# Kernel tuning notes

Measured on AMD Instinct MI355X. Metric: run time of the kernel, lower is better.

Reference implementation:

```python
import jax, jax.numpy as jnp
import numpy as np

Nu, Ni, Nb, Nc, Nr = 100000, 100000, 5000, 2000, 50000
E, Eb, Ec, Er = 600000, 100000, 200000, 400000
D, L = 64, 50


def _seg_softmax(logits, seg, n):
    m = jax.ops.segment_max(logits, seg, num_segments=n)
    e = jnp.exp(logits - m[seg])
    s = jax.ops.segment_sum(e, seg, num_segments=n)
    return e / (s[seg] + 1e-9)


def setup_inputs():
    key = jax.random.key(0)
    ks = jax.random.split(key, 32)
    f = lambda i, shape, s=0.05: jax.random.normal(ks[i], shape, jnp.float32) * s
    return dict(
        user_h=f(0, (Nu, D), 1.0), item_h=f(1, (Ni, D), 1.0),
        brand_feat=f(2, (Nb, D), 1.0), cat_feat=f(3, (Nc, D), 1.0), rel_feat=f(4, (Nr, D), 1.0),
        Wu=f(5, (D, D)), Wi=f(6, (D, D)), Wb=f(7, (D, D)), Wc=f(8, (D, D)), Wr=f(9, (D, D)),
        Wg_u=f(10, (2 * D, D)), Wg_i=f(11, (2 * D, D)),
        u_pos=f(12, (L, D)), u_pos_k=f(13, (L, D)), i_pos=f(14, (L, D)), i_pos_k=f(15, (L, D)),
        basis_freq=jnp.asarray(1.0 / 10 ** np.linspace(0, 9, D), jnp.float32),
        phase=jnp.zeros((D,), jnp.float32),
        Wr0=f(16, (D, D)), Wr1=f(17, (D, D)), Wr2=f(18, (D, D)),
        e_time=jax.random.uniform(ks[19], (E,), jnp.float32),
        e_iid=jax.random.randint(ks[20], (E,), 0, Ni),
        e_uid=jax.random.randint(ks[21], (E,), 0, Nu),
        pos_u=jax.random.randint(ks[22], (E,), 0, L),
        pos_i=jax.random.randint(ks[23], (E,), 0, L),
        eb_src=jax.random.randint(ks[24], (Eb,), 0, Nb),
        eb_dst=jax.random.randint(ks[25], (Eb,), 0, Ni),
        ec_src=jax.random.randint(ks[26], (Ec,), 0, Nc),
        ec_dst=jax.random.randint(ks[27], (Ec,), 0, Ni),
        er_src=jax.random.randint(ks[28], (Er,), 0, Nr),
        er_dst=jax.random.randint(ks[29], (Er,), 0, Ni),
    )


def reference(user_h, item_h, brand_feat, cat_feat, rel_feat, Wu, Wi, Wb, Wc, Wr,
              Wg_u, Wg_i, u_pos, u_pos_k, i_pos, i_pos_k, basis_freq, phase,
              Wr0, Wr1, Wr2, e_time,
              e_iid, e_uid, pos_u, pos_i, eb_src, eb_dst, ec_src, ec_dst, er_src, er_dst):
    sqrtD = jnp.sqrt(jnp.float32(D))
    # relation-specific linear transforms (user_weight / item_weight / att_trans)
    uh = user_h @ Wu                      # [Nu,D]
    ih = item_h @ Wi                      # [Ni,D]
    bf = brand_feat @ Wb
    cf = cat_feat @ Wc
    rf = rel_feat @ Wr
    # TimeEncode harmonic features per purchase edge
    t_enc = jnp.cos(e_time[:, None] * basis_freq[None, :] + phase[None, :])  # [E,D]

    hi = ih[e_iid]                        # [E,D] item-side gather
    hu = uh[e_uid]                        # [E,D] user-side gather

    # ---- user aggregation: 'orgat' long-term (pos + time aware) + 'att' short-term ----
    k_long = hi + u_pos_k[pos_u] + t_enc
    a_long = _seg_softmax(jnp.sum(k_long * hu, -1) / sqrtD, e_uid, Nu)
    h_long_u = jax.ops.segment_sum(a_long[:, None] * (hi + u_pos[pos_u]), e_uid, num_segments=Nu)
    a_short = _seg_softmax(jnp.sum(hi * hu, -1) / sqrtD, e_uid, Nu)
    h_short_u = jax.ops.segment_sum(a_short[:, None] * hi, e_uid, num_segments=Nu)
    user_new = jnp.concatenate([h_long_u, h_short_u], -1) @ Wg_u  # agg_gate_u

    # ---- item aggregation from users (symmetric) ----
    k_long_i = hu + i_pos_k[pos_i] + t_enc
    b_long = _seg_softmax(jnp.sum(k_long_i * hi, -1) / sqrtD, e_iid, Ni)
    h_long_i = jax.ops.segment_sum(b_long[:, None] * (hu + i_pos[pos_i]), e_iid, num_segments=Ni)
    b_short = _seg_softmax(jnp.sum(hu * hi, -1) / sqrtD, e_iid, Ni)
    h_short_i = jax.ops.segment_sum(b_short[:, None] * hu, e_iid, num_segments=Ni)
    item_new = jnp.concatenate([h_long_i, h_short_i], -1) @ Wg_i  # agg_gate_i

    # ---- relation mean aggregation onto items (reduce_trans per relation) ----
    def mean_agg(feat, src, dst, W):
        s = jax.ops.segment_sum(feat[src], dst, num_segments=Ni)
        c = jax.ops.segment_sum(jnp.ones(src.shape, feat.dtype), dst, num_segments=Ni)
        return (s / jnp.maximum(c, 1.0)[:, None]) @ W

    item_new = item_new + mean_agg(bf, eb_src, eb_dst, Wr0) \
                        + mean_agg(cf, ec_src, ec_dst, Wr1) \
                        + mean_agg(rf, er_src, er_dst, Wr2)

    # residual update: elu(now + old)
    user_out = jax.nn.elu(user_new + user_h)
    item_out = jax.nn.elu(item_new + item_h)
    return user_out, item_out
```

## Files before the change

### kernel.cpp

```cpp
#include <hip/hip_runtime.h>
#include <hip/hip_bf16.h>
#include <hip/hip_fp16.h>

typedef __hip_bfloat16 bf16_t;

#define NU 100000
#define NI 100000
#define NB_ 5000
#define NC_ 2000
#define NR_ 50000
#define NE 600000
#define NEB 100000
#define NEC 200000
#define NER 400000
#define NPERM (2 * NE + NEB + NEC + NER)
#define NRELE (NEB + NEC + NER)
#define NALL (NE + NRELE)
#define SCAN_N (2 * NU + NI + 1)
#define SCAN_CHUNK 2048
#define SCAN_NCHUNK ((SCAN_N + SCAN_CHUNK - 1) / SCAN_CHUNK)
#define PBLK 8192
#define RBLK ((NRELE + 255) / 256)

#define AGS 136
#define RLS 68

typedef __attribute__((ext_vector_type(8))) short short8;
typedef __attribute__((ext_vector_type(4))) short short4v;
typedef __attribute__((ext_vector_type(4))) float f32x4;

__device__ __forceinline__ float b2f(bf16_t x) { return __bfloat162float(x); }
__device__ __forceinline__ float sane(float x) { return isfinite(x) ? x : 0.f; }
__device__ __forceinline__ unsigned short f2bu(float x) {
    union { bf16_t b; unsigned short u; } c; c.b = __float2bfloat16(x); return c.u;
}

__device__ __forceinline__ float ldf(const void* p, size_t i, int f32) {
    return f32 ? ((const float*)p)[i] : __bfloat162float(((const bf16_t*)p)[i]);
}
__device__ __forceinline__ void stf(void* p, size_t i, float v, int f32) {
    if (f32) ((float*)p)[i] = v;
    else     ((bf16_t*)p)[i] = __float2bfloat16(v);
}

__device__ __forceinline__ f32x4 bf4(const bf16_t* p) {
    short4v s = *(const short4v*)p;
    f32x4 r;
#pragma unroll
    for (int q = 0; q < 4; ++q)
        r[q] = __uint_as_float(((unsigned)(unsigned short)s[q]) << 16);
    return r;
}
__device__ __forceinline__ f32x4 ldf4(const void* p, size_t i, int f32) {
    if (f32) return *(const f32x4*)((const float*)p + i);
    return bf4((const bf16_t*)p + i);
}

__device__ __forceinline__ void bf8(const bf16_t* p, float* o) {
    short8 s = *(const short8*)p;
#pragma unroll
    for (int q = 0; q < 8; ++q)
        o[q] = __uint_as_float(((unsigned)(unsigned short)s[q]) << 16);
}
__device__ __forceinline__ void ldf8(const void* p, size_t i, int f32, float* o) {
    if (f32) {
        f32x4 a = *(const f32x4*)((const float*)p + i);
        f32x4 b = *(const f32x4*)((const float*)p + i + 4);
#pragma unroll
        for (int q = 0; q < 4; ++q) { o[q] = a[q]; o[4 + q] = b[q]; }
    } else {
        bf8((const bf16_t*)p + i, o);
    }
}

__global__ void detect_dtype(const unsigned int* w, int* flag) {
    if (threadIdx.x == 0 && blockIdx.x == 0) *flag = (w[0] == 0x3F800000u) ? 1 : 0;
}

__global__ __launch_bounds__(256) void combine_w(
    const void* Wb, const void* Wr0,
    const void* Wc, const void* Wr1,
    const void* Wr, const void* Wr2,
    const void* Wg_u, const void* Wg_i,
    bf16_t* out, bf16_t* wgsw, const int* flagp) {
    int f = *flagp;
    if (blockIdx.x < 48) {
        int mat = blockIdx.x >> 4;
        int sub = blockIdx.x & 15;
        const void* A = mat == 0 ? Wb : (mat == 1 ? Wc : Wr);
        const void* B = mat == 0 ? Wr0 : (mat == 1 ? Wr1 : Wr2);
        int idx = sub * 256 + threadIdx.x;
        int i = idx >> 6, j = idx & 63;
        float acc = 0.f;
        for (int k = 0; k < 64; ++k)
            acc = fmaf(ldf(A, i * 64 + k, f), ldf(B, k * 64 + j, f), acc);
        out[(size_t)mat * 4096 + idx] = __float2bfloat16(acc);
    } else {
        int t = (blockIdx.x - 48) * 256 + threadIdx.x;
        int mat = t >> 13;
        int i = t & 8191;
        int j = i & 7, ln = (i >> 3) & 63, p = i >> 9;
        int kk4 = p >> 2, n0t = p & 3;
        int srow = kk4 * 32 + (ln >> 4) * 8 + j;
        int scol = n0t * 16 + (ln & 15);
        const void* src = mat ? Wg_i : Wg_u;
        wgsw[(size_t)mat * 8192 + i] = __float2bfloat16(ldf(src, (size_t)srow * 64 + scol, f));
    }
}

struct GSeg {
    const void* A; const void* W; void* out;
    int M; int a_internal; int w_internal;
};

__global__ __launch_bounds__(256) void gemm_multi(
    GSeg s0, GSeg s1, GSeg s2, GSeg s3, GSeg s4,
    int nseg, const int* __restrict__ flagp) {
    const int K = 64;
    __shared__ short WL[64 * 64];
    int f = *flagp;
    int nt0 = (s0.M + 63) >> 6;
    int nt1 = (nseg > 1) ? ((s1.M + 63) >> 6) : 0;
    int nt2 = (nseg > 2) ? ((s2.M + 63) >> 6) : 0;
    int nt3 = (nseg > 3) ? ((s3.M + 63) >> 6) : 0;
    int nt4 = (nseg > 4) ? ((s4.M + 63) >> 6) : 0;
    int c0 = nt0, c1 = c0 + nt1, c2 = c1 + nt2, c3 = c2 + nt3;
    int ntT = c3 + nt4;
    int lane = threadIdx.x & 63;
    int wv = threadIdx.x >> 6;
    int q = lane >> 4, nl = lane & 15;
    int staged = -1;
    for (int tile = blockIdx.x; tile < ntT; tile += gridDim.x) {
        int sidx, t_in;
        if (tile < c0) { sidx = 0; t_in = tile; }
        else if (tile < c1) { sidx = 1; t_in = tile - c0; }
        else if (tile < c2) { sidx = 2; t_in = tile - c1; }
        else if (tile < c3) { sidx = 3; t_in = tile - c2; }
        else { sidx = 4; t_in = tile - c3; }
        const void* A; const void* W; void* out; int M, a_int, w_int;
        if (sidx == 0)      { A = s0.A; W = s0.W; out = s0.out; M = s0.M; a_int = s0.a_internal; w_int = s0.w_internal; }
        else if (sidx == 1) { A = s1.A; W = s1.W; out = s1.out; M = s1.M; a_int = s1.a_internal; w_int = s1.w_internal; }
        else if (sidx == 2) { A = s2.A; W = s2.W; out = s2.out; M = s2.M; a_int = s2.a_internal; w_int = s2.w_internal; }
        else if (sidx == 3) { A = s3.A; W = s3.W; out = s3.out; M = s3.M; a_int = s3.a_internal; w_int = s3.w_internal; }
        else                { A = s4.A; W = s4.W; out = s4.out; M = s4.M; a_int = s4.a_internal; w_int = s4.w_internal; }
        if (sidx != staged) {
            __syncthreads();
            int w_f32 = w_int ? 0 : f;
            for (int i = threadIdx.x; i < K * 64; i += 256) {
                int j = i & 7, ln = (i >> 3) & 63, p = i >> 9;
                int kk4 = p >> 2, n0t = p & 3;
                int srow = kk4 * 32 + (ln >> 4) * 8 + j;
                int scol = n0t * 16 + (ln & 15);
                float wvv = w_f32 ? ((const float*)W)[srow * 64 + scol]
                                  : b2f(((const bf16_t*)W)[srow * 64 + scol]);
                WL[i] = (short)f2bu(wvv);
            }
            __syncthreads();
            staged = sidx;
        }
        int m0 = t_in * 64 + wv * 16;
        if (m0 < M) {
            int a_f32 = a_int ? 0 : f;
            int arow = m0 + nl; if (arow >= M) arow = M - 1;
            f32x4 acc[4];
#pragma unroll
            for (int t = 0; t < 4; ++t) acc[t] = (f32x4){0.f, 0.f, 0.f, 0.f};
            for (int kk4 = 0; kk4 < 2; ++kk4) {
                short8 af;
                size_t abase = (size_t)arow * K + kk4 * 32 + q * 8;
                if (a_f32) {
                    const f32x4* ap = (const f32x4*)((const float*)A + abase);
                    f32x4 x0 = ap[0], x1 = ap[1];
#pragma unroll
                    for (int j = 0; j < 4; ++j) {
                        af[j] = (short)f2bu(x0[j]);
                        af[4 + j] = (short)f2bu(x1[j]);
                    }
                } else {
                    af = *(const short8*)((const bf16_t*)A + abase);
                }
#pragma unroll
                for (int n0t = 0; n0t < 4; ++n0t) {
                    short8 bfr = *(const short8*)&WL[(((kk4 << 2) + n0t) * 64 + lane) * 8];
                    acc[n0t] = __builtin_amdgcn_mfma_f32_16x16x32_bf16(af, bfr, acc[n0t], 0, 0, 0);
                }
            }
#pragma unroll
            for (int n0t = 0; n0t < 4; ++n0t) {
#pragma unroll
                for (int r = 0; r < 4; ++r) {
                    int row = m0 + q * 4 + r;
                    if (row >= M) continue;
                    int col = n0t * 16 + nl;
                    ((bf16_t*)out)[(size_t)row * 64 + col] = __float2bfloat16(acc[n0t][r]);
                }
            }
        }
    }
}

__global__ __launch_bounds__(256) void hist_all(
    const int* __restrict__ e_uid, const int* __restrict__ e_iid,
    const int* __restrict__ eb_dst, const int* __restrict__ ec_dst,
    const int* __restrict__ er_dst, int* __restrict__ deg) {
    int t = blockIdx.x * blockDim.x + threadIdx.x;
    if (t < NE) {
        atomicAdd(deg + e_uid[t], 1);
        atomicAdd(deg + NU + e_iid[t], 1);
    } else if (t < NE + NEB) {
        atomicAdd(deg + 2 * NU + eb_dst[t - NE], 1);
    } else if (t < NE + NEB + NEC) {
        atomicAdd(deg + 2 * NU + ec_dst[t - NE - NEB], 1);
    } else if (t < NALL) {
        atomicAdd(deg + 2 * NU + er_dst[t - NE - NEB - NEC], 1);
    }
}

__global__ __launch_bounds__(256) void scan1(const int* __restrict__ deg,
                                             int* __restrict__ off,
                                             int* __restrict__ ctot) {
    __shared__ int part[256];
    int base = blockIdx.x * SCAN_CHUNK + threadIdx.x * 8;
    int v[8]; int s = 0;
#pragma unroll
    for (int k = 0; k < 8; ++k) {
        int idx = base + k;
        v[k] = s;
        s += (idx < SCAN_N) ? deg[idx] : 0;
    }
    part[threadIdx.x] = s;
    __syncthreads();
    for (int o = 1; o < 256; o <<= 1) {
        int t = (threadIdx.x >= o) ? part[threadIdx.x - o] : 0;
        __syncthreads();
        part[threadIdx.x] += t;
        __syncthreads();
    }
    int texc = (threadIdx.x == 0) ? 0 : part[threadIdx.x - 1];
#pragma unroll
    for (int k = 0; k < 8; ++k) {
        int idx = base + k;
        if (idx < SCAN_N) off[idx] = texc + v[k];
    }
    if (threadIdx.x == 255) ctot[blockIdx.x] = part[255];
}
__global__ __launch_bounds__(256) void scan23(int* __restrict__ off,
                                              const int* __restrict__ ctot,
                                              int* __restrict__ cur) {
    __shared__ int part[256];
    int t = threadIdx.x;
    part[t] = (t < SCAN_NCHUNK) ? ctot[t] : 0;
    __syncthreads();
    for (int o = 1; o < 256; o <<= 1) {
        int x = (t >= o) ? part[t - o] : 0;
        __syncthreads();
        part[t] += x;
        __syncthreads();
    }
    int add = blockIdx.x ? part[blockIdx.x - 1] : 0;
    int base = blockIdx.x * SCAN_CHUNK + t;
#pragma unroll
    for (int k = 0; k < 8; ++k) {
        int idx = base + k * 256;
        if (idx < SCAN_N) { int v = off[idx] + add; off[idx] = v; cur[idx] = v; }
    }
}

__global__ __launch_bounds__(256) void edges_fused(
    const bf16_t* __restrict__ uh, const bf16_t* __restrict__ ih,
    const void* __restrict__ u_pos_k, const void* __restrict__ i_pos_k,
    const void* __restrict__ basis_freq, const void* __restrict__ phase_,
    const void* __restrict__ e_time,
    const int* __restrict__ e_uid, const int* __restrict__ e_iid,
    const int* __restrict__ pos_u, const int* __restrict__ pos_i,
    const int* __restrict__ eb_src, const int* __restrict__ eb_dst,
    const int* __restrict__ ec_src, const int* __restrict__ ec_dst,
    const int* __restrict__ er_src, const int* __restrict__ er_dst,
    int* __restrict__ cur, uint2* __restrict__ perm, const int* flagp) {
    if (blockIdx.x >= PBLK) {
        int t = (blockIdx.x - PBLK) * 256 + threadIdx.x;
        if (t < NEB) {
            int p = atomicAdd(cur + 2 * NU + eb_dst[t], 1);
            perm[p] = make_uint2((unsigned)eb_src[t], 0u);
        } else if (t < NEB + NEC) {
            int e = t - NEB;
            int p = atomicAdd(cur + 2 * NU + ec_dst[e], 1);
            perm[p] = make_uint2((unsigned)(ec_src[e] + NB_) | (1u << 17), 0u);
        } else if (t < NRELE) {
            int e = t - NEB - NEC;
            int p = atomicAdd(cur + 2 * NU + er_dst[e], 1);
            perm[p] = make_uint2((unsigned)(er_src[e] + NB_ + NC_) | (2u << 17), 0u);
        }
        return;
    }
    int f = *flagp;
    int lane = threadIdx.x & 63;
    int g = lane >> 3, l = lane & 7;
    float bfv[8], phv[8];
    ldf8(basis_freq, (size_t)l * 8, f, bfv);
    ldf8(phase_, (size_t)l * 8, f, phv);
    int w = (blockIdx.x * 256 + threadIdx.x) >> 6;
    const int NWAVE = PBLK * 4;
    for (int eb = w; eb < NE / 8; eb += NWAVE) {
        int e = eb * 8 + g;
        int uid = e_uid[e], iid = e_iid[e], pu = pos_u[e], pi = pos_i[e];
        float t = ldf(e_time, e, f);
        float hu[8], hi[8], pku[8], pki[8];
        bf8(uh + (size_t)uid * 64 + l * 8, hu);
        bf8(ih + (size_t)iid * 64 + l * 8, hi);
        ldf8(u_pos_k, (size_t)pu * 64 + l * 8, f, pku);
        ldf8(i_pos_k, (size_t)pi * 64 + l * 8, f, pki);
        float d_lu = 0.f, d_sh = 0.f, d_li = 0.f;
#pragma unroll
        for (int qq = 0; qq < 8; ++qq) {
            float te = __cosf(fmaf(t, bfv[qq], phv[qq]));
            d_lu = fmaf(hi[qq] + pku[qq] + te, hu[qq], d_lu);
            d_sh = fmaf(hi[qq], hu[qq], d_sh);
            d_li = fmaf(hu[qq] + pki[qq] + te, hi[qq], d_li);
        }
#pragma unroll
        for (int o = 1; o < 8; o <<= 1) {
            d_lu += __shfl_xor(d_lu, o, 64);
            d_sh += __shfl_xor(d_sh, o, 64);
            d_li += __shfl_xor(d_li, o, 64);
        }
        if (l == 0) {
            float p_lu = __expf(fminf(d_lu * 0.125f, 10.f));
            float p_sh = __expf(fminf(d_sh * 0.125f, 10.f));
            unsigned pkt_u = (unsigned)__half_as_ushort(__float2half(p_lu))
                           | ((unsigned)__half_as_ushort(__float2half(p_sh)) << 16);
            int s1 = atomicAdd(cur + uid, 1);
            perm[s1] = make_uint2((unsigned)iid | ((unsigned)pu << 17), pkt_u);
        } else if (l == 1) {
            float p_li = __expf(fminf(d_li * 0.125f, 10.f));
            float p_sh = __expf(fminf(d_sh * 0.125f, 10.f));
            unsigned pkt_i = (unsigned)__half_as_ushort(__float2half(p_li))
                           | ((unsigned)__half_as_ushort(__float2half(p_sh)) << 16);
            int s2 = atomicAdd(cur + NU + iid, 1);
            perm[s2] = make_uint2((unsigned)uid | ((unsigned)pi << 17), pkt_i);
        }
    }
}

__global__ __launch_bounds__(256) void gather_gemm(
    const bf16_t* __restrict__ uh, const bf16_t* __restrict__ ih,
    const void* __restrict__ u_pos, const void* __restrict__ i_pos,
    const int* __restrict__ off, const uint2* __restrict__ perm,
    const bf16_t* __restrict__ fW, const bf16_t* __restrict__ wgsw,
    const void* __restrict__ user_h, const void* __restrict__ item_h,
    void* __restrict__ d_out, const int* flagp) {
    __shared__ short AG[16 * AGS];
    __shared__ short RL[16 * RLS];
    int f = *flagp;
    int lane = threadIdx.x & 63;
    int l = lane & 15;
    int gb = lane & 48;
    int l4 = l * 4;
    int grp = threadIdx.x >> 4;
    int v0 = blockIdx.x * 16;
    int v = v0 + grp;
    int phase = v >= NU;
    int vtx = phase ? v - NU : v;
    const bf16_t* other = phase ? uh : ih;
    const void* pv = phase ? i_pos : u_pos;
    int j0 = off[v], j1 = off[v + 1];
    f32x4 a0 = (f32x4){0.f, 0.f, 0.f, 0.f}, a1 = a0;
    float s1 = 0.f, s2 = 0.f;
    for (int cb = j0; cb < j1; cb += 16) {
        int m = j1 - cb; if (m > 16) m = 16;
        uint2 pay = make_uint2(0u, 0u);
        if (l < m) pay = perm[cb + l];
        unsigned px0 = (unsigned)__shfl((int)pay.x, gb, 64);
        unsigned py0 = (unsigned)__shfl((int)pay.y, gb, 64);
        f32x4 ho0 = bf4(other + (size_t)(px0 & 0x1FFFF) * 64 + l4);
        f32x4 pv0 = ldf4(pv, (size_t)((px0 >> 17) & 63) * 64 + l4, f);
        for (int k = 0; k < m; ++k) {
            unsigned px1 = 0, py1 = 0;
            f32x4 ho1 = (f32x4){0.f, 0.f, 0.f, 0.f}, pv1 = ho1;
            if (k + 1 < m) {
                px1 = (unsigned)__shfl((int)pay.x, gb + k + 1, 64);
                py1 = (unsigned)__shfl((int)pay.y, gb + k + 1, 64);
                ho1 = bf4(other + (size_t)(px1 & 0x1FFFF) * 64 + l4);
                pv1 = ldf4(pv, (size_t)((px1 >> 17) & 63) * 64 + l4, f);
            }
            float p1 = __half2float(__ushort_as_half((unsigned short)(py0 & 0xFFFF)));
            float p2 = __half2float(__ushort_as_half((unsigned short)(py0 >> 16)));
#pragma unroll
            for (int q = 0; q < 4; ++q) {
                a0[q] = fmaf(p1, ho0[q] + pv0[q], a0[q]);
                a1[q] = fmaf(p2, ho0[q], a1[q]);
            }
            s1 += p1; s2 += p2;
            px0 = px1; py0 = py1; ho0 = ho1; pv0 = pv1;
        }
    }
    float inv1 = 1.f / (s1 + 1e-9f), inv2 = 1.f / (s2 + 1e-9f);
    {
        short4v o0, o1;
#pragma unroll
        for (int q = 0; q < 4; ++q) {
            o0[q] = (short)f2bu(a0[q] * inv1);
            o1[q] = (short)f2bu(a1[q] * inv2);
        }
        *(short4v*)&AG[grp * AGS + l4] = o0;
        *(short4v*)&AG[grp * AGS + 64 + l4] = o1;
    }
    if (phase) {
        f32x4 r0 = (f32x4){0.f, 0.f, 0.f, 0.f}, r1 = r0, r2 = r0;
        int c0 = 0, c1 = 0, c2 = 0;
        int k0 = off[2 * NU + vtx], k1 = off[2 * NU + vtx + 1];
        for (int cb = k0; cb < k1; cb += 16) {
            int m = k1 - cb; if (m > 16) m = 16;
            unsigned px = 0u;
            if (l < m) px = perm[cb + l].x;
            unsigned u0 = (unsigned)__shfl((int)px, gb, 64);
            f32x4 fv0 = bf4(fW + (size_t)(u0 & 0x1FFFF) * 64 + l4);
            for (int k = 0; k < m; ++k) {
                unsigned u1 = 0;
                f32x4 fv1 = (f32x4){0.f, 0.f, 0.f, 0.f};
                if (k + 1 < m) {
                    u1 = (unsigned)__shfl((int)px, gb + k + 1, 64);
                    fv1 = bf4(fW + (size_t)(u1 & 0x1FFFF) * 64 + l4);
                }
                int r = (u0 >> 17) & 3;
                if (r == 0) {
#pragma unroll
                    for (int q = 0; q < 4; ++q) r0[q] += fv0[q];
                    c0++;
                } else if (r == 1) {
#pragma unroll
                    for (int q = 0; q < 4; ++q) r1[q] += fv0[q];
                    c1++;
                } else {
#pragma unroll
                    for (int q = 0; q < 4; ++q) r2[q] += fv0[q];
                    c2++;
                }
                u0 = u1; fv0 = fv1;
            }
        }
        float w0 = 1.f / fmaxf((float)c0, 1.f);
        float w1 = 1.f / fmaxf((float)c1, 1.f);
        float w2 = 1.f / fmaxf((float)c2, 1.f);
        short4v ro;
#pragma unroll
        for (int q = 0; q < 4; ++q)
            ro[q] = (short)f2bu(r0[q] * w0 + r1[q] * w1 + r2[q] * w2);
        *(short4v*)&RL[grp * RLS + l4] = ro;
    }
    __syncthreads();
    int wv = threadIdx.x >> 6;
    int q = lane >> 4, nl = lane & 15;
    const bf16_t* wg = wgsw + (phase ? 8192 : 0);
    f32x4 acc = (f32x4){0.f, 0.f, 0.f, 0.f};
#pragma unroll
    for (int kk = 0; kk < 4; ++kk) {
        short8 af = *(const short8*)&AG[nl * AGS + kk * 32 + q * 8];
        short8 bfr = *(const short8*)&wg[(((kk << 2) + wv) * 64 + lane) * 8];
        acc = __builtin_amdgcn_mfma_f32_16x16x32_bf16(af, bfr, acc, 0, 0, 0);
    }
    const void* hext = phase ? item_h : user_h;
    int hbase = phase ? v0 - NU : v0;
#pragma unroll
    for (int r = 0; r < 4; ++r) {
        int row = q * 4 + r;
        int col = wv * 16 + nl;
        float val = acc[r];
        val += ldf(hext, (size_t)(hbase + row) * 64 + col, f);
        if (phase) val += b2f(((const bf16_t*)RL)[row * RLS + col]);
        val = val > 0.f ? val : expm1f(val);
        stf(d_out, (size_t)(v0 + row) * 64 + col, sane(val), f);
    }
}

extern "C" void kernel_launch(void* const* d_in, const int* in_sizes, int n_in,
                              void* d_out, int out_size, void* d_ws, size_t ws_size,
                              hipStream_t stream) {
    const void* user_h     = d_in[0];
    const void* item_h     = d_in[1];
    const void* brand_feat = d_in[2];
    const void* cat_feat   = d_in[3];
    const void* rel_feat   = d_in[4];
    const void* Wu   = d_in[5];
    const void* Wi   = d_in[6];
    const void* Wb   = d_in[7];
    const void* Wc   = d_in[8];
    const void* Wr   = d_in[9];
    const void* Wg_u = d_in[10];
    const void* Wg_i = d_in[11];
    const void* u_pos   = d_in[12];
    const void* u_pos_k = d_in[13];
    const void* i_pos   = d_in[14];
    const void* i_pos_k = d_in[15];
    const void* basis_freq = d_in[16];
    const void* phase      = d_in[17];
    const void* Wr0 = d_in[18];
    const void* Wr1 = d_in[19];
    const void* Wr2 = d_in[20];
    const void* e_time = d_in[21];
    const int* e_iid  = (const int*)d_in[22];
    const int* e_uid  = (const int*)d_in[23];
    const int* pos_u  = (const int*)d_in[24];
    const int* pos_i  = (const int*)d_in[25];
    const int* eb_src = (const int*)d_in[26];
    const int* eb_dst = (const int*)d_in[27];
    const int* ec_src = (const int*)d_in[28];
    const int* ec_dst = (const int*)d_in[29];
    const int* er_src = (const int*)d_in[30];
    const int* er_dst = (const int*)d_in[31];

    char* base = (char*)d_ws;
    size_t off_b = 0;
    auto alloc = [&](size_t bytes) { size_t p = off_b; off_b = (off_b + bytes + 511) & ~(size_t)511; return p; };
    size_t o_flag  = alloc(512);
    size_t o_uh    = alloc((size_t)NU * 64 * 2);
    size_t o_ih    = alloc((size_t)NI * 64 * 2);
    size_t o_fW    = alloc((size_t)(NB_ + NC_ + NR_ + 64) * 64 * 2);
    size_t o_wcomb = alloc((size_t)3 * 4096 * 2);
    size_t o_wgsw  = alloc((size_t)2 * 8192 * 2);
    size_t o_deg   = alloc((size_t)SCAN_N * 4);
    size_t o_off   = alloc((size_t)SCAN_N * 4);
    size_t o_cur   = alloc((size_t)SCAN_N * 4);
    size_t o_ctot  = alloc((size_t)SCAN_NCHUNK * 4);
    size_t o_perm  = alloc((size_t)NPERM * 8);

    int*    flagp = (int*)(base + o_flag);
    bf16_t* uh    = (bf16_t*)(base + o_uh);
    bf16_t* ih    = (bf16_t*)(base + o_ih);
    bf16_t* fW    = (bf16_t*)(base + o_fW);
    bf16_t* wcomb = (bf16_t*)(base + o_wcomb);
    bf16_t* wgsw  = (bf16_t*)(base + o_wgsw);
    int*    deg   = (int*)(base + o_deg);
    int*    offp  = (int*)(base + o_off);
    int*    cur   = (int*)(base + o_cur);
    int*    ctot  = (int*)(base + o_ctot);
    uint2*  perm  = (uint2*)(base + o_perm);

    hipMemsetAsync(deg, 0, (size_t)SCAN_N * 4, stream);
    detect_dtype<<<1, 64, 0, stream>>>((const unsigned int*)basis_freq, flagp);

    combine_w<<<112, 256, 0, stream>>>(Wb, Wr0, Wc, Wr1, Wr, Wr2, Wg_u, Wg_i,
                                       wcomb, wgsw, flagp);

    {
        GSeg su = {user_h,     Wu,           uh,                            NU,  0, 0};
        GSeg si = {item_h,     Wi,           ih,                            NI,  0, 0};
        GSeg sb = {brand_feat, wcomb,        fW,                            NB_, 0, 1};
        GSeg sc = {cat_feat,   wcomb + 4096, fW + (size_t)NB_ * 64,         NC_, 0, 1};
        GSeg sr = {rel_feat,   wcomb + 8192, fW + (size_t)(NB_ + NC_) * 64, NR_, 0, 1};
        gemm_multi<<<1024, 256, 0, stream>>>(su, si, sb, sc, sr, 5, flagp);
    }

    hist_all<<<(NALL + 255) / 256, 256, 0, stream>>>(e_uid, e_iid, eb_dst, ec_dst, er_dst, deg);
    scan1<<<SCAN_NCHUNK, 256, 0, stream>>>(deg, offp, ctot);
    scan23<<<SCAN_NCHUNK, 256, 0, stream>>>(offp, ctot, cur);

    edges_fused<<<PBLK + RBLK, 256, 0, stream>>>(uh, ih, u_pos_k, i_pos_k, basis_freq, phase,
                                                 e_time, e_uid, e_iid, pos_u, pos_i,
                                                 eb_src, eb_dst, ec_src, ec_dst,
                                                 er_src, er_dst, cur, perm, flagp);

    gather_gemm<<<(NU + NI) / 16, 256, 0, stream>>>(uh, ih, u_pos, i_pos, offp, perm, fW,
                                                    wgsw, user_h, item_h, d_out, flagp);
}
```

Baseline: 514.2 us.

## Fuse degree histogram into GEMM launch and issue slot atomics earlier

Merges the degree-histogram kernel into the multi-segment GEMM launch as extra blocks, so the atomics run alongside the GEMM tiles and one launch is dropped. In the edge kernel, the per-edge slot atomicAdd now issues right after the indices are loaded, so its latency overlaps the feature gathers and dot products. It also halves the edge-pass block count. The histogram blocks now grid-stride over edges and compete with the GEMM for CU resources.

```diff
diff --git a/kernel.cpp b/kernel.cpp
--- a/kernel.cpp
+++ b/kernel.cpp
@@ -19,8 +19,10 @@
 #define SCAN_N (2 * NU + NI + 1)
 #define SCAN_CHUNK 2048
 #define SCAN_NCHUNK ((SCAN_N + SCAN_CHUNK - 1) / SCAN_CHUNK)
-#define PBLK 8192
+#define PBLK 4096
 #define RBLK ((NRELE + 255) / 256)
+#define GEMM_BLKS 1024
+#define HIST_BLKS 2048
 
 #define AGS 136
 #define RLS 68
@@ -113,9 +115,29 @@
     int M; int a_internal; int w_internal;
 };
 
-__global__ __launch_bounds__(256) void gemm_multi(
+__global__ __launch_bounds__(256) void gemm_hist(
     GSeg s0, GSeg s1, GSeg s2, GSeg s3, GSeg s4,
-    int nseg, const int* __restrict__ flagp) {
+    int nseg, const int* __restrict__ flagp,
+    const int* __restrict__ e_uid, const int* __restrict__ e_iid,
+    const int* __restrict__ eb_dst, const int* __restrict__ ec_dst,
+    const int* __restrict__ er_dst, int* __restrict__ deg) {
+    if (blockIdx.x >= GEMM_BLKS) {
+        int tid = (blockIdx.x - GEMM_BLKS) * 256 + threadIdx.x;
+        const int nthr = HIST_BLKS * 256;
+        for (int t = tid; t < NALL; t += nthr) {
+            if (t < NE) {
+                atomicAdd(deg + e_uid[t], 1);
+                atomicAdd(deg + NU + e_iid[t], 1);
+            } else if (t < NE + NEB) {
+                atomicAdd(deg + 2 * NU + eb_dst[t - NE], 1);
+            } else if (t < NE + NEB + NEC) {
+                atomicAdd(deg + 2 * NU + ec_dst[t - NE - NEB], 1);
+            } else {
+                atomicAdd(deg + 2 * NU + er_dst[t - NE - NEB - NEC], 1);
+            }
+        }
+        return;
+    }
     const int K = 64;
     __shared__ short WL[64 * 64];
     int f = *flagp;
@@ -130,7 +152,7 @@
     int wv = threadIdx.x >> 6;
     int q = lane >> 4, nl = lane & 15;
     int staged = -1;
-    for (int tile = blockIdx.x; tile < ntT; tile += gridDim.x) {
+    for (int tile = blockIdx.x; tile < ntT; tile += GEMM_BLKS) {
         int sidx, t_in;
         if (tile < c0) { sidx = 0; t_in = tile; }
         else if (tile < c1) { sidx = 1; t_in = tile - c0; }
@@ -196,23 +218,6 @@
                 }
             }
         }
-    }
-}
-
-__global__ __launch_bounds__(256) void hist_all(
-    const int* __restrict__ e_uid, const int* __restrict__ e_iid,
-    const int* __restrict__ eb_dst, const int* __restrict__ ec_dst,
-    const int* __restrict__ er_dst, int* __restrict__ deg) {
-    int t = blockIdx.x * blockDim.x + threadIdx.x;
-    if (t < NE) {
-        atomicAdd(deg + e_uid[t], 1);
-        atomicAdd(deg + NU + e_iid[t], 1);
-    } else if (t < NE + NEB) {
-        atomicAdd(deg + 2 * NU + eb_dst[t - NE], 1);
-    } else if (t < NE + NEB + NEC) {
-        atomicAdd(deg + 2 * NU + ec_dst[t - NE - NEB], 1);
-    } else if (t < NALL) {
-        atomicAdd(deg + 2 * NU + er_dst[t - NE - NEB - NEC], 1);
     }
 }
 
@@ -304,6 +309,9 @@
     for (int eb = w; eb < NE / 8; eb += NWAVE) {
         int e = eb * 8 + g;
         int uid = e_uid[e], iid = e_iid[e], pu = pos_u[e], pi = pos_i[e];
+        int slot = 0;
+        if (l == 0)      slot = atomicAdd(cur + uid, 1);
+        else if (l == 1) slot = atomicAdd(cur + NU + iid, 1);
         float t = ldf(e_time, e, f);
         float hu[8], hi[8], pku[8], pki[8];
         bf8(uh + (size_t)uid * 64 + l * 8, hu);
@@ -329,15 +337,13 @@
             float p_sh = __expf(fminf(d_sh * 0.125f, 10.f));
             unsigned pkt_u = (unsigned)__half_as_ushort(__float2half(p_lu))
                            | ((unsigned)__half_as_ushort(__float2half(p_sh)) << 16);
-            int s1 = atomicAdd(cur + uid, 1);
-            perm[s1] = make_uint2((unsigned)iid | ((unsigned)pu << 17), pkt_u);
+            perm[slot] = make_uint2((unsigned)iid | ((unsigned)pu << 17), pkt_u);
         } else if (l == 1) {
             float p_li = __expf(fminf(d_li * 0.125f, 10.f));
             float p_sh = __expf(fminf(d_sh * 0.125f, 10.f));
             unsigned pkt_i = (unsigned)__half_as_ushort(__float2half(p_li))
                            | ((unsigned)__half_as_ushort(__float2half(p_sh)) << 16);
-            int s2 = atomicAdd(cur + NU + iid, 1);
-            perm[s2] = make_uint2((unsigned)uid | ((unsigned)pi << 17), pkt_i);
+            perm[slot] = make_uint2((unsigned)uid | ((unsigned)pi << 17), pkt_i);
         }
     }
 }
@@ -548,10 +554,11 @@
         GSeg sb = {brand_feat, wcomb,        fW,                            NB_, 0, 1};
         GSeg sc = {cat_feat,   wcomb + 4096, fW + (size_t)NB_ * 64,         NC_, 0, 1};
         GSeg sr = {rel_feat,   wcomb + 8192, fW + (size_t)(NB_ + NC_) * 64, NR_, 0, 1};
-        gemm_multi<<<1024, 256, 0, stream>>>(su, si, sb, sc, sr, 5, flagp);
-    }
-
-    hist_all<<<(NALL + 255) / 256, 256, 0, stream>>>(e_uid, e_iid, eb_dst, ec_dst, er_dst, deg);
+        gemm_hist<<<GEMM_BLKS + HIST_BLKS, 256, 0, stream>>>(
+            su, si, sb, sc, sr, 5, flagp,
+            e_uid, e_iid, eb_dst, ec_dst, er_dst, deg);
+    }
+
     scan1<<<SCAN_NCHUNK, 256, 0, stream>>>(deg, offp, ctot);
     scan23<<<SCAN_NCHUNK, 256, 0, stream>>>(offp, ctot, cur);
 
```

Result: faster. 498.8 us (-3.0%).
